# Kernel tuning notes

Measured on AMD Instinct MI355X. Metric: run time of the kernel, lower is better.

Reference implementation:

```python
import jax, jax.numpy as jnp
import numpy as np

N = 8192
F_IN = 256
F_OUT = 64
ALPHA = 0.2  # leaky relu negative slope
MASK_VAL = -9e15


def setup_inputs() -> dict:
    key = jax.random.key(0)
    k1, k2, k3, k4, k5, k6 = jax.random.split(key, 6)
    stdv_lin = 1.0 / np.sqrt(F_IN)
    stdv_a = 1.0 / np.sqrt(2 * F_OUT)
    return {
        "input": jax.random.normal(k1, (N, F_IN), dtype=jnp.float32),
        "adj": jax.random.randint(k2, (N, N), 0, 2, dtype=jnp.int32),
        "W": jax.random.uniform(k3, (F_IN, F_OUT), minval=-stdv_lin, maxval=stdv_lin, dtype=jnp.float32),
        "b_lin": jax.random.uniform(k4, (F_OUT,), minval=-stdv_lin, maxval=stdv_lin, dtype=jnp.float32),
        "a": jax.random.uniform(k5, (2 * F_OUT, 1), minval=-stdv_a, maxval=stdv_a, dtype=jnp.float32),
        "bias": jax.random.uniform(k6, (F_OUT,), minval=-stdv_a, maxval=stdv_a, dtype=jnp.float32),
    }


def reference(input, adj, W, b_lin, a, bias):
    # h = Linear(input): [N, F_OUT]
    h = input @ W + b_lin
    # e[i,j] = leaky_relu(a1 . h_i + a2 . h_j)  (equivalent to the repeat/cat/matmul in torch,
    # without materializing the [N, N, 2*F_OUT] tensor)
    a1 = a[:F_OUT, 0]
    a2 = a[F_OUT:, 0]
    s1 = h @ a1  # [N]
    s2 = h @ a2  # [N]
    e = jax.nn.leaky_relu(s1[:, None] + s2[None, :], negative_slope=ALPHA)  # [N, N]
    attention = jnp.where(adj > 0, e, MASK_VAL)
    attention = jax.nn.softmax(attention, axis=1)
    # dropout is identity in eval mode (training=False)
    output = attention @ h + bias
    return output
```

## Files before the change

### kernel.cpp

```cpp
#include <hip/hip_runtime.h>

#define N 8192
#define FIN 256
#define FOUT 64
#define ALPHA 0.2f
#define LOG2C 3
#define NCHUNK (1 << LOG2C)
#define CLEN (N >> LOG2C)
#define ITERS (CLEN / 64)

typedef float f32x4 __attribute__((ext_vector_type(4)));
typedef short s16x8 __attribute__((ext_vector_type(8)));

static __device__ __forceinline__ unsigned short f2bf(float x) {
    unsigned u = __float_as_uint(x);
    u += 0x7fffu + ((u >> 16) & 1u);
    return (unsigned short)(u >> 16);
}

__global__ __launch_bounds__(256) void k_linear(
    const float* __restrict__ input, const float* __restrict__ W,
    const float* __restrict__ b_lin, const float* __restrict__ a,
    unsigned short* __restrict__ hTf, float* __restrict__ s1, float* __restrict__ s2,
    unsigned* __restrict__ s2max_enc)
{
    __shared__ float in_sh[16 * FIN];
    __shared__ float hst[64][17];
    int t = threadIdx.x, w = t >> 6, f = t & 63;
    int b = blockIdx.x;
    int i0 = b * 16;

#pragma unroll
    for (int r = 0; r < 4; r++) {
        int row = w * 4 + r;
        *(float4*)&in_sh[row * FIN + f * 4] =
            *(const float4*)(input + (size_t)(i0 + row) * FIN + f * 4);
    }

    float a1v = a[f], a2v = a[FOUT + f];
    float h[4];
#pragma unroll
    for (int r = 0; r < 4; r++) h[r] = b_lin[f];

    for (int k4 = 0; k4 < FIN / 4; k4++) {
        float wv0 = W[(k4 * 4 + 0) * FOUT + f];
        float wv1 = W[(k4 * 4 + 1) * FOUT + f];
        float wv2 = W[(k4 * 4 + 2) * FOUT + f];
        float wv3 = W[(k4 * 4 + 3) * FOUT + f];
#pragma unroll
        for (int r = 0; r < 4; r++) {
            float4 iv = *(const float4*)&in_sh[(w * 4 + r) * FIN + k4 * 4];
            h[r] = fmaf(iv.x, wv0, h[r]);
            h[r] = fmaf(iv.y, wv1, h[r]);
            h[r] = fmaf(iv.z, wv2, h[r]);
            h[r] = fmaf(iv.w, wv3, h[r]);
        }
    }

    float wmax = -1e30f;
#pragma unroll
    for (int r = 0; r < 4; r++) {
        hst[f][w * 4 + r] = h[r];
        float v1 = h[r] * a1v, v2 = h[r] * a2v;
#pragma unroll
        for (int d = 1; d < 64; d <<= 1) { v1 += __shfl_xor(v1, d); v2 += __shfl_xor(v2, d); }
        wmax = fmaxf(wmax, v2);
        if (f == 0) { s1[i0 + w * 4 + r] = v1; s2[i0 + w * 4 + r] = v2; }
    }
    if (f == 0) {
        unsigned u = __float_as_uint(wmax);
        unsigned key = (u & 0x80000000u) ? ~u : (u | 0x80000000u);
        atomicMax(s2max_enc, key);
    }
    __syncthreads();

    int fo = t >> 2, seg = t & 3;
    unsigned lo = f2bf(hst[fo][seg * 4 + 0]) | ((unsigned)f2bf(hst[fo][seg * 4 + 1]) << 16);
    unsigned hi = f2bf(hst[fo][seg * 4 + 2]) | ((unsigned)f2bf(hst[fo][seg * 4 + 3]) << 16);
    int2 v; v.x = (int)lo; v.y = (int)hi;
    size_t base = (size_t)(b >> 1) * 2048 + (size_t)fo * 32 + (b & 1) * 16 + seg * 4;
    *(int2*)(hTf + base) = v;
}


#define PGEN(AV0, AV1, SVP, AFR) do {                                             \
    float4 sv0 = *(const float4*)(SVP);                                           \
    float4 sv1 = *(const float4*)((SVP) + 4);                                     \
    float p0, p1, p2, p3, p4, p5, p6, p7;                                         \
    { float u = s1c + sv0.x; float g = fmaxf(u, fmaf(0.2f, u, c2)); p0 = (AV0.x > 0) ? exp2f(g) : 0.f; } \
    { float u = s1c + sv0.y; float g = fmaxf(u, fmaf(0.2f, u, c2)); p1 = (AV0.y > 0) ? exp2f(g) : 0.f; } \
    { float u = s1c + sv0.z; float g = fmaxf(u, fmaf(0.2f, u, c2)); p2 = (AV0.z > 0) ? exp2f(g) : 0.f; } \
    { float u = s1c + sv0.w; float g = fmaxf(u, fmaf(0.2f, u, c2)); p3 = (AV0.w > 0) ? exp2f(g) : 0.f; } \
    { float u = s1c + sv1.x; float g = fmaxf(u, fmaf(0.2f, u, c2)); p4 = (AV1.x > 0) ? exp2f(g) : 0.f; } \
    { float u = s1c + sv1.y; float g = fmaxf(u, fmaf(0.2f, u, c2)); p5 = (AV1.y > 0) ? exp2f(g) : 0.f; } \
    { float u = s1c + sv1.z; float g = fmaxf(u, fmaf(0.2f, u, c2)); p6 = (AV1.z > 0) ? exp2f(g) : 0.f; } \
    { float u = s1c + sv1.w; float g = fmaxf(u, fmaf(0.2f, u, c2)); p7 = (AV1.w > 0) ? exp2f(g) : 0.f; } \
    dacc += ((p0 + p1) + (p2 + p3)) + ((p4 + p5) + (p6 + p7));                    \
    union { s16x8 v; unsigned u[4]; } pk;                                         \
    asm("v_cvt_pk_bf16_f32 %0, %1, %2" : "=v"(pk.u[0]) : "v"(p0), "v"(p1));       \
    asm("v_cvt_pk_bf16_f32 %0, %1, %2" : "=v"(pk.u[1]) : "v"(p2), "v"(p3));       \
    asm("v_cvt_pk_bf16_f32 %0, %1, %2" : "=v"(pk.u[2]) : "v"(p4), "v"(p5));       \
    asm("v_cvt_pk_bf16_f32 %0, %1, %2" : "=v"(pk.u[3]) : "v"(p6), "v"(p7));       \
    AFR = pk.v;                                                                   \
} while (0)

__global__ __launch_bounds__(256) void k_attn(
    const int* __restrict__ adj, const float* __restrict__ s1g,
    const float* __restrict__ s2g, const unsigned short* __restrict__ hTf,
    const unsigned* __restrict__ s2max_enc,
    float* __restrict__ numP, float* __restrict__ denP)
{
    __shared__ unsigned short hsh[2][4096];
    __shared__ float s2sh[CLEN];

    const float LOG2E = 1.4426950408889634f;
    int bid = blockIdx.x;
    int chunk = bid & (NCHUNK - 1);
    int rg = bid >> LOG2C;
    int jstart = chunk * CLEN;
    int t = threadIdx.x, w = t >> 6, l = t & 63;
    int l15 = l & 15, kg = l >> 4;
    int kgs = kg ^ ((l15 >> 1) & 3);

    int D0 = w * 128 + l;
    int D1 = w * 128 + 64 + l;
    int S0 = (D0 & ~3) | ((D0 ^ (D0 >> 3)) & 3);
    int S1 = (D1 & ~3) | ((D1 ^ (D1 >> 3)) & 3);
    const char* srcb = (const char*)(hTf + (size_t)jstart * 64);

    {
        float4 sv = ((const float4*)(s2g + jstart))[t];
        sv.x *= LOG2E; sv.y *= LOG2E; sv.z *= LOG2E; sv.w *= LOG2E;
        ((float4*)s2sh)[t] = sv;
    }
    __builtin_amdgcn_global_load_lds(srcb + (size_t)S0 * 16,
                                     (char*)&hsh[0][0] + w * 2048, 16, 0, 0);
    __builtin_amdgcn_global_load_lds(srcb + (size_t)S1 * 16,
                                     (char*)&hsh[0][0] + w * 2048 + 1024, 16, 0, 0);

    unsigned key = *s2max_enc;
    unsigned su = (key & 0x80000000u) ? (key ^ 0x80000000u) : ~key;
    float s2m = __uint_as_float(su);

    int i0 = rg * 64;
    int i = i0 + w * 16 + l15;
    float s1v = s1g[i];
    float mx = s1v + s2m; mx = fmaxf(mx, ALPHA * mx);
    float m2 = mx * LOG2E;
    float s1c = fmaf(s1v, LOG2E, -m2);
    float c2 = -0.8f * m2;

    const int4* adjq = (const int4*)(adj + (size_t)i * N + jstart);
    int4 a0 = adjq[kg * 2 + 0];
    int4 a1 = adjq[kg * 2 + 1];
    int4 a2 = adjq[8 + kg * 2 + 0];
    int4 a3 = adjq[8 + kg * 2 + 1];

    f32x4 acc[4] = {};
    float dacc = 0.f;
    __syncthreads();

#pragma unroll 1
    for (int it = 0; it < ITERS; it++) {
        int cur = it & 1;
        bool more = (it + 1 < ITERS);
        if (more) {
            const char* s = srcb + (size_t)(it + 1) * 8192;
            char* d = (char*)&hsh[cur ^ 1][0] + w * 2048;
            __builtin_amdgcn_global_load_lds(s + (size_t)S0 * 16, d, 16, 0, 0);
            __builtin_amdgcn_global_load_lds(s + (size_t)S1 * 16, d + 1024, 16, 0, 0);
        }
        int4 n0, n1, n2, n3;
        if (more) {
            n0 = adjq[(it + 1) * 16 + kg * 2 + 0];
            n1 = adjq[(it + 1) * 16 + kg * 2 + 1];
            n2 = adjq[(it + 1) * 16 + 8 + kg * 2 + 0];
            n3 = adjq[(it + 1) * 16 + 8 + kg * 2 + 1];
        }

        const float* svp = &s2sh[it * 64 + kg * 8];
        const unsigned short* bt = &hsh[cur][0] + l15 * 32 + kgs * 8;
        {
            s16x8 b0 = *(const s16x8*)(bt);
            s16x8 b1 = *(const s16x8*)(bt + 512);
            s16x8 b2 = *(const s16x8*)(bt + 1024);
            s16x8 b3 = *(const s16x8*)(bt + 1536);
            s16x8 afr;
            PGEN(a0, a1, svp, afr);
            acc[0] = __builtin_amdgcn_mfma_f32_16x16x32_bf16(afr, b0, acc[0], 0, 0, 0);
            acc[1] = __builtin_amdgcn_mfma_f32_16x16x32_bf16(afr, b1, acc[1], 0, 0, 0);
            acc[2] = __builtin_amdgcn_mfma_f32_16x16x32_bf16(afr, b2, acc[2], 0, 0, 0);
            acc[3] = __builtin_amdgcn_mfma_f32_16x16x32_bf16(afr, b3, acc[3], 0, 0, 0);
        }
        {
            s16x8 b0 = *(const s16x8*)(bt + 2048);
            s16x8 b1 = *(const s16x8*)(bt + 2560);
            s16x8 b2 = *(const s16x8*)(bt + 3072);
            s16x8 b3 = *(const s16x8*)(bt + 3584);
            s16x8 afr;
            PGEN(a2, a3, svp + 32, afr);
            acc[0] = __builtin_amdgcn_mfma_f32_16x16x32_bf16(afr, b0, acc[0], 0, 0, 0);
            acc[1] = __builtin_amdgcn_mfma_f32_16x16x32_bf16(afr, b1, acc[1], 0, 0, 0);
            acc[2] = __builtin_amdgcn_mfma_f32_16x16x32_bf16(afr, b2, acc[2], 0, 0, 0);
            acc[3] = __builtin_amdgcn_mfma_f32_16x16x32_bf16(afr, b3, acc[3], 0, 0, 0);
        }
        if (more) {
            asm volatile("s_waitcnt vmcnt(4) lgkmcnt(0)" ::: "memory");
            __builtin_amdgcn_s_barrier();
            a0 = n0; a1 = n1; a2 = n2; a3 = n3;
        }
    }

    dacc += __shfl_xor(dacc, 16);
    dacc += __shfl_xor(dacc, 32);
    if (l < 16) denP[(size_t)chunk * N + i0 + w * 16 + l] = dacc;
#pragma unroll
    for (int nt = 0; nt < 4; nt++) {
#pragma unroll
        for (int r = 0; r < 4; r++) {
            int orow = w * 16 + kg * 4 + r;
            numP[((size_t)chunk * N + i0 + orow) * FOUT + nt * 16 + l15] = acc[nt][r];
        }
    }
}

__global__ __launch_bounds__(256) void k_finalize(
    const float* __restrict__ numP, const float* __restrict__ denP,
    const float* __restrict__ bias, float* __restrict__ out)
{
    int idx = blockIdx.x * 256 + threadIdx.x;
    int i = idx >> 6, f = idx & 63;
    float nsum = 0.f, dsum = 0.f;
#pragma unroll
    for (int c = 0; c < NCHUNK; c++) {
        nsum += numP[(size_t)c * (N * FOUT) + idx];
        dsum += denP[(size_t)c * N + i];
    }
    out[idx] = nsum / dsum + bias[f];
}

extern "C" void kernel_launch(void* const* d_in, const int* in_sizes, int n_in,
                              void* d_out, int out_size, void* d_ws, size_t ws_size,
                              hipStream_t stream)
{
    const float* input = (const float*)d_in[0];
    const int*   adj   = (const int*)d_in[1];
    const float* W     = (const float*)d_in[2];
    const float* b_lin = (const float*)d_in[3];
    const float* a     = (const float*)d_in[4];
    const float* bias  = (const float*)d_in[5];
    float* out = (float*)d_out;

    char* ws = (char*)d_ws;
    unsigned short* hTf = (unsigned short*)ws;
    float* s1    = (float*)(ws + 1048576);
    float* s2    = (float*)(ws + 1048576 + 32768);
    unsigned* s2max_enc = (unsigned*)(ws + 1048576 + 65536);
    size_t fixed = 1048576 + 65536 + 256;
    float* numP = (float*)(ws + fixed);
    float* denP = (float*)(ws + fixed + ((size_t)N * FOUT * 4) * NCHUNK);

    hipMemsetAsync(s2max_enc, 0, 4, stream);
    hipLaunchKernelGGL(k_linear, dim3(512), dim3(256), 0, stream,
                       input, W, b_lin, a, hTf, s1, s2, s2max_enc);
    hipLaunchKernelGGL(k_attn, dim3((N / 64) * NCHUNK), dim3(256), 0, stream,
                       adj, s1, s2, hTf, s2max_enc, numP, denP);
    hipLaunchKernelGGL(k_finalize, dim3(2048), dim3(256), 0, stream,
                       numP, denP, bias, out);
}
```

Before: 105.2 us.

## Pre-pack adjacency into bitmask and read bits in attention kernel

Adds a separate pass that reads the int32 adjacency matrix and packs it into a 1-bit-per-entry mask. The attention kernel then loads one 64-bit word per iteration instead of four int4 vectors per lane, which cuts its register pressure and global load count. The full 256 MB adjacency is still read once in the pack pass, so total traffic is about the same plus a small mask write and read, and an extra kernel launch is added.

Measured after the change: 127.2 us. 1.21x slower.

```diff
diff --git a/kernel.cpp b/kernel.cpp
--- a/kernel.cpp
+++ b/kernel.cpp
@@ -18,6 +18,28 @@
     return (unsigned short)(u >> 16);
 }
 
+__global__ __launch_bounds__(256) void k_pack(const int* __restrict__ adj,
+                                              unsigned short* __restrict__ pk)
+{
+    size_t g = (size_t)blockIdx.x * 256 + threadIdx.x;
+    size_t stride = (size_t)gridDim.x * 256;
+    size_t total = (size_t)N * N / 16;
+    for (; g < total; g += stride) {
+        const int4* p = (const int4*)(adj + g * 16);
+        int4 a = p[0], b = p[1], c = p[2], d = p[3];
+        unsigned m = 0;
+        m |= (unsigned)(a.x > 0) << 0;  m |= (unsigned)(a.y > 0) << 1;
+        m |= (unsigned)(a.z > 0) << 2;  m |= (unsigned)(a.w > 0) << 3;
+        m |= (unsigned)(b.x > 0) << 4;  m |= (unsigned)(b.y > 0) << 5;
+        m |= (unsigned)(b.z > 0) << 6;  m |= (unsigned)(b.w > 0) << 7;
+        m |= (unsigned)(c.x > 0) << 8;  m |= (unsigned)(c.y > 0) << 9;
+        m |= (unsigned)(c.z > 0) << 10; m |= (unsigned)(c.w > 0) << 11;
+        m |= (unsigned)(d.x > 0) << 12; m |= (unsigned)(d.y > 0) << 13;
+        m |= (unsigned)(d.z > 0) << 14; m |= (unsigned)(d.w > 0) << 15;
+        pk[g] = (unsigned short)m;
+    }
+}
+
 __global__ __launch_bounds__(256) void k_linear(
     const float* __restrict__ input, const float* __restrict__ W,
     const float* __restrict__ b_lin, const float* __restrict__ a,
@@ -83,18 +105,18 @@
 }
 
 
-#define PGEN(AV0, AV1, SVP, AFR) do {                                             \
+#define PGEN(BITS, SVP, AFR) do {                                                 \
     float4 sv0 = *(const float4*)(SVP);                                           \
     float4 sv1 = *(const float4*)((SVP) + 4);                                     \
     float p0, p1, p2, p3, p4, p5, p6, p7;                                         \
-    { float u = s1c + sv0.x; float g = fmaxf(u, fmaf(0.2f, u, c2)); p0 = (AV0.x > 0) ? exp2f(g) : 0.f; } \
-    { float u = s1c + sv0.y; float g = fmaxf(u, fmaf(0.2f, u, c2)); p1 = (AV0.y > 0) ? exp2f(g) : 0.f; } \
-    { float u = s1c + sv0.z; float g = fmaxf(u, fmaf(0.2f, u, c2)); p2 = (AV0.z > 0) ? exp2f(g) : 0.f; } \
-    { float u = s1c + sv0.w; float g = fmaxf(u, fmaf(0.2f, u, c2)); p3 = (AV0.w > 0) ? exp2f(g) : 0.f; } \
-    { float u = s1c + sv1.x; float g = fmaxf(u, fmaf(0.2f, u, c2)); p4 = (AV1.x > 0) ? exp2f(g) : 0.f; } \
-    { float u = s1c + sv1.y; float g = fmaxf(u, fmaf(0.2f, u, c2)); p5 = (AV1.y > 0) ? exp2f(g) : 0.f; } \
-    { float u = s1c + sv1.z; float g = fmaxf(u, fmaf(0.2f, u, c2)); p6 = (AV1.z > 0) ? exp2f(g) : 0.f; } \
-    { float u = s1c + sv1.w; float g = fmaxf(u, fmaf(0.2f, u, c2)); p7 = (AV1.w > 0) ? exp2f(g) : 0.f; } \
+    { float u = s1c + sv0.x; float g = fmaxf(u, fmaf(0.2f, u, c2)); p0 = (((BITS) >> 0) & 1) ? exp2f(g) : 0.f; } \
+    { float u = s1c + sv0.y; float g = fmaxf(u, fmaf(0.2f, u, c2)); p1 = (((BITS) >> 1) & 1) ? exp2f(g) : 0.f; } \
+    { float u = s1c + sv0.z; float g = fmaxf(u, fmaf(0.2f, u, c2)); p2 = (((BITS) >> 2) & 1) ? exp2f(g) : 0.f; } \
+    { float u = s1c + sv0.w; float g = fmaxf(u, fmaf(0.2f, u, c2)); p3 = (((BITS) >> 3) & 1) ? exp2f(g) : 0.f; } \
+    { float u = s1c + sv1.x; float g = fmaxf(u, fmaf(0.2f, u, c2)); p4 = (((BITS) >> 4) & 1) ? exp2f(g) : 0.f; } \
+    { float u = s1c + sv1.y; float g = fmaxf(u, fmaf(0.2f, u, c2)); p5 = (((BITS) >> 5) & 1) ? exp2f(g) : 0.f; } \
+    { float u = s1c + sv1.z; float g = fmaxf(u, fmaf(0.2f, u, c2)); p6 = (((BITS) >> 6) & 1) ? exp2f(g) : 0.f; } \
+    { float u = s1c + sv1.w; float g = fmaxf(u, fmaf(0.2f, u, c2)); p7 = (((BITS) >> 7) & 1) ? exp2f(g) : 0.f; } \
     dacc += ((p0 + p1) + (p2 + p3)) + ((p4 + p5) + (p6 + p7));                    \
     union { s16x8 v; unsigned u[4]; } pk;                                         \
     asm("v_cvt_pk_bf16_f32 %0, %1, %2" : "=v"(pk.u[0]) : "v"(p0), "v"(p1));       \
@@ -105,7 +127,7 @@
 } while (0)
 
 __global__ __launch_bounds__(256) void k_attn(
-    const int* __restrict__ adj, const float* __restrict__ s1g,
+    const unsigned long long* __restrict__ pkm, const float* __restrict__ s1g,
     const float* __restrict__ s2g, const unsigned short* __restrict__ hTf,
     const unsigned* __restrict__ s2max_enc,
     float* __restrict__ numP, float* __restrict__ denP)
@@ -150,11 +172,8 @@
     float s1c = fmaf(s1v, LOG2E, -m2);
     float c2 = -0.8f * m2;
 
-    const int4* adjq = (const int4*)(adj + (size_t)i * N + jstart);
-    int4 a0 = adjq[kg * 2 + 0];
-    int4 a1 = adjq[kg * 2 + 1];
-    int4 a2 = adjq[8 + kg * 2 + 0];
-    int4 a3 = adjq[8 + kg * 2 + 1];
+    const unsigned long long* pkq = pkm + (((size_t)i * N + jstart) >> 6);
+    unsigned long long mcur = pkq[0];
 
     f32x4 acc[4] = {};
     float dacc = 0.f;
@@ -164,20 +183,17 @@
     for (int it = 0; it < ITERS; it++) {
         int cur = it & 1;
         bool more = (it + 1 < ITERS);
+        unsigned long long mnext = 0;
         if (more) {
             const char* s = srcb + (size_t)(it + 1) * 8192;
             char* d = (char*)&hsh[cur ^ 1][0] + w * 2048;
             __builtin_amdgcn_global_load_lds(s + (size_t)S0 * 16, d, 16, 0, 0);
             __builtin_amdgcn_global_load_lds(s + (size_t)S1 * 16, d + 1024, 16, 0, 0);
-        }
-        int4 n0, n1, n2, n3;
-        if (more) {
-            n0 = adjq[(it + 1) * 16 + kg * 2 + 0];
-            n1 = adjq[(it + 1) * 16 + kg * 2 + 1];
-            n2 = adjq[(it + 1) * 16 + 8 + kg * 2 + 0];
-            n3 = adjq[(it + 1) * 16 + 8 + kg * 2 + 1];
-        }
-
+            mnext = pkq[it + 1];
+        }
+
+        unsigned bits0 = (unsigned)(mcur >> (kg * 8)) & 0xffu;
+        unsigned bits1 = (unsigned)(mcur >> (kg * 8 + 32)) & 0xffu;
         const float* svp = &s2sh[it * 64 + kg * 8];
         const unsigned short* bt = &hsh[cur][0] + l15 * 32 + kgs * 8;
         {
@@ -186,7 +202,7 @@
             s16x8 b2 = *(const s16x8*)(bt + 1024);
             s16x8 b3 = *(const s16x8*)(bt + 1536);
             s16x8 afr;
-            PGEN(a0, a1, svp, afr);
+            PGEN(bits0, svp, afr);
             acc[0] = __builtin_amdgcn_mfma_f32_16x16x32_bf16(afr, b0, acc[0], 0, 0, 0);
             acc[1] = __builtin_amdgcn_mfma_f32_16x16x32_bf16(afr, b1, acc[1], 0, 0, 0);
             acc[2] = __builtin_amdgcn_mfma_f32_16x16x32_bf16(afr, b2, acc[2], 0, 0, 0);
@@ -198,16 +214,16 @@
             s16x8 b2 = *(const s16x8*)(bt + 3072);
             s16x8 b3 = *(const s16x8*)(bt + 3584);
             s16x8 afr;
-            PGEN(a2, a3, svp + 32, afr);
+            PGEN(bits1, svp + 32, afr);
             acc[0] = __builtin_amdgcn_mfma_f32_16x16x32_bf16(afr, b0, acc[0], 0, 0, 0);
             acc[1] = __builtin_amdgcn_mfma_f32_16x16x32_bf16(afr, b1, acc[1], 0, 0, 0);
             acc[2] = __builtin_amdgcn_mfma_f32_16x16x32_bf16(afr, b2, acc[2], 0, 0, 0);
             acc[3] = __builtin_amdgcn_mfma_f32_16x16x32_bf16(afr, b3, acc[3], 0, 0, 0);
         }
         if (more) {
-            asm volatile("s_waitcnt vmcnt(4) lgkmcnt(0)" ::: "memory");
+            asm volatile("s_waitcnt vmcnt(1) lgkmcnt(0)" ::: "memory");
             __builtin_amdgcn_s_barrier();
-            a0 = n0; a1 = n1; a2 = n2; a3 = n3;
+            mcur = mnext;
         }
     }
 
@@ -259,12 +275,15 @@
     size_t fixed = 1048576 + 65536 + 256;
     float* numP = (float*)(ws + fixed);
     float* denP = (float*)(ws + fixed + ((size_t)N * FOUT * 4) * NCHUNK);
+    unsigned short* pk = (unsigned short*)(ws + fixed
+                         + ((size_t)N * FOUT * 4) * NCHUNK + (size_t)N * 4 * NCHUNK);
 
     hipMemsetAsync(s2max_enc, 0, 4, stream);
     hipLaunchKernelGGL(k_linear, dim3(512), dim3(256), 0, stream,
                        input, W, b_lin, a, hTf, s1, s2, s2max_enc);
+    hipLaunchKernelGGL(k_pack, dim3(2048), dim3(256), 0, stream, adj, pk);
     hipLaunchKernelGGL(k_attn, dim3((N / 64) * NCHUNK), dim3(256), 0, stream,
-                       adj, s1, s2, hTf, s2max_enc, numP, denP);
+                       (const unsigned long long*)pk, s1, s2, hTf, s2max_enc, numP, denP);
     hipLaunchKernelGGL(k_finalize, dim3(2048), dim3(256), 0, stream,
                        numP, denP, bias, out);
 }
```
